# Kernel tuning notes

Measured on AMD Instinct MI355X. Metric: run time of the kernel, lower is better.

## Reference

```python
import jax, jax.numpy as jnp
import numpy as np

NUM_REQS = 8192
MAX_NUM_REQS = 16384
NUM_TOKENS = 16_777_216
MAX_CTX = 32768


def setup_inputs() -> dict:
    key = jax.random.key(0)
    k1, k2, k3 = jax.random.split(key, 3)
    # cumulative query start offsets: sorted, qsl[0]=0, qsl[-1]=NUM_TOKENS
    inner = jnp.sort(jax.random.randint(k1, (NUM_REQS - 1,), 0, NUM_TOKENS, dtype=jnp.int32))
    query_start_loc = jnp.concatenate([
        jnp.zeros((1,), jnp.int32), inner, jnp.full((1,), NUM_TOKENS, jnp.int32)
    ])
    idx_mapping = jax.random.randint(k2, (NUM_REQS,), 0, MAX_NUM_REQS, dtype=jnp.int32)
    num_computed_tokens = jax.random.randint(k3, (MAX_NUM_REQS,), 0, MAX_CTX, dtype=jnp.int32)
    pos = jnp.zeros((NUM_TOKENS,), jnp.int32)       # output buffer
    seq_lens = jnp.zeros((MAX_NUM_REQS,), jnp.int32)  # output buffer
    return {
        "idx_mapping": idx_mapping,
        "query_start_loc": query_start_loc,
        "num_computed_tokens": num_computed_tokens,
        "pos": pos,
        "seq_lens": seq_lens,
    }


def reference(idx_mapping, query_start_loc, num_computed_tokens, pos, seq_lens):
    num_reqs = idx_mapping.shape[0]            # static
    max_num_reqs = seq_lens.shape[0]           # static
    num_tokens = pos.shape[0]                  # static; == query_start_loc[-1] by construction

    # per-request query lengths and gathered computed-token counts
    query_lens = query_start_loc[1:] - query_start_loc[:-1]      # [num_reqs]
    nct = num_computed_tokens[idx_mapping]                       # [num_reqs]

    # seq_lens: [0:num_reqs] = nct + query_len, [num_reqs:] = 0
    seq_lens_out = jnp.zeros((max_num_reqs,), seq_lens.dtype).at[:num_reqs].set(
        (nct + query_lens).astype(seq_lens.dtype)
    )

    # pos: for each token t, find its owning request via searchsorted over
    # the ragged offsets, then pos[t] = nct[req] + (t - start[req]).
    t = jnp.arange(num_tokens, dtype=query_start_loc.dtype)      # [num_tokens]
    req = jnp.searchsorted(query_start_loc, t, side="right") - 1 # [num_tokens]
    req = jnp.clip(req, 0, num_reqs - 1)
    pos_out = (nct[req] + (t - query_start_loc[req])).astype(pos.dtype)

    return pos_out, seq_lens_out
```

## Files before the change

### kernel.cpp

```cpp
#include <hip/hip_runtime.h>


#define TPB 256
#define TILE_TOK 1024
#define SEQ_PER_BLOCK (TPB * 4)

typedef int vint4 __attribute__((ext_vector_type(4)));

__global__ __launch_bounds__(TPB) void fused_kernel(
    const int* __restrict__ idx_mapping,
    const int* __restrict__ qsl,
    const int* __restrict__ nct,
    int* __restrict__ pos_out,
    int* __restrict__ seq_out,
    int num_reqs, int max_num_reqs, int num_tokens,
    int pos_blocks)
{
    int b = blockIdx.x;

    if (b >= pos_blocks) {
        int i = (b - pos_blocks) * SEQ_PER_BLOCK + (int)threadIdx.x * 4;
        if (i >= max_num_reqs) return;
        vint4 v;
        #pragma unroll
        for (int k = 0; k < 4; ++k) {
            int idx = i + k;
            int val = 0;
            if (idx < num_reqs)
                val = nct[idx_mapping[idx]] + (qsl[idx + 1] - qsl[idx]);
            v[k] = val;
        }
        if (i + 4 <= max_num_reqs) {
            *(vint4*)(seq_out + i) = v;
        } else {
            for (int k = 0; k < max_num_reqs - i; ++k) seq_out[i + k] = v[k];
        }
        return;
    }

    int t = b * TILE_TOK + (int)threadIdx.x * 4;
    int tc = (t < num_tokens) ? t : (num_tokens - 1);

    int l = 0, h = num_reqs + 1;
    while (h - l > 1) {
        int mid = (l + h) >> 1;
        if (qsl[mid] <= tc) l = mid; else h = mid;
    }
    int r = l;
    int next = qsl[r + 1];
    int base = nct[idx_mapping[r]] - qsl[r];

    vint4 v;
    #pragma unroll
    for (int k = 0; k < 4; ++k) {
        int tk = t + k;
        while (tk >= next && r < num_reqs - 1) {
            ++r;
            next = qsl[r + 1];
            base = nct[idx_mapping[r]] - qsl[r];
        }
        v[k] = base + tk;
    }

    if (t + 4 <= num_tokens) {
        __builtin_nontemporal_store(v, (vint4*)(pos_out + t));
    } else {
        for (int k = 0; k < num_tokens - t; ++k) pos_out[t + k] = v[k];
    }
}

extern "C" void kernel_launch(void* const* d_in, const int* in_sizes, int n_in,
                              void* d_out, int out_size, void* d_ws, size_t ws_size,
                              hipStream_t stream) {
    const int* idx_mapping = (const int*)d_in[0];
    const int* qsl         = (const int*)d_in[1];
    const int* nct         = (const int*)d_in[2];

    int num_reqs     = in_sizes[0];
    int max_num_reqs = in_sizes[2];
    int num_tokens   = in_sizes[3];

    int* out = (int*)d_out;
    int* pos_out = out;
    int* seq_out = out + num_tokens;

    int pos_blocks = (int)(((long long)num_tokens + TILE_TOK - 1) / TILE_TOK);
    int seq_blocks = (max_num_reqs + SEQ_PER_BLOCK - 1) / SEQ_PER_BLOCK;

    fused_kernel<<<dim3(pos_blocks + seq_blocks), dim3(TPB), 0, stream>>>(
        idx_mapping, qsl, nct, pos_out, seq_out,
        num_reqs, max_num_reqs, num_tokens, pos_blocks);
}
```

Baseline: 142.2 us.

## Assign one block per request and drop per-token binary search

Work for the pos output is now split per request instead of per fixed token tile. Each block reads its request's start, end and base offset once, then strides over that request's tokens with aligned vector nontemporal stores, plus scalar head and tail stores. This removes the dependent binary search over query_start_loc that every thread ran, and the inner request-advance loop. In exchange, blocks get uneven amounts of work because request lengths vary, and misaligned head and tail elements use scalar stores.

```diff
diff --git a/kernel.cpp b/kernel.cpp
--- a/kernel.cpp
+++ b/kernel.cpp
@@ -2,7 +2,6 @@
 
 
 #define TPB 256
-#define TILE_TOK 1024
 #define SEQ_PER_BLOCK (TPB * 4)
 
 typedef int vint4 __attribute__((ext_vector_type(4)));
@@ -13,13 +12,13 @@
     const int* __restrict__ nct,
     int* __restrict__ pos_out,
     int* __restrict__ seq_out,
-    int num_reqs, int max_num_reqs, int num_tokens,
-    int pos_blocks)
+    int num_reqs, int max_num_reqs)
 {
     int b = blockIdx.x;
+    int tid = (int)threadIdx.x;
 
-    if (b >= pos_blocks) {
-        int i = (b - pos_blocks) * SEQ_PER_BLOCK + (int)threadIdx.x * 4;
+    if (b >= num_reqs) {
+        int i = (b - num_reqs) * SEQ_PER_BLOCK + tid * 4;
         if (i >= max_num_reqs) return;
         vint4 v;
         #pragma unroll
@@ -38,35 +37,25 @@
         return;
     }
 
-    int t = b * TILE_TOK + (int)threadIdx.x * 4;
-    int tc = (t < num_tokens) ? t : (num_tokens - 1);
+    int r = b;
+    int start = qsl[r];
+    int end   = qsl[r + 1];
+    if (start >= end) return;
+    int base  = nct[idx_mapping[r]] - start;
 
-    int l = 0, h = num_reqs + 1;
-    while (h - l > 1) {
-        int mid = (l + h) >> 1;
-        if (qsl[mid] <= tc) l = mid; else h = mid;
-    }
-    int r = l;
-    int next = qsl[r + 1];
-    int base = nct[idx_mapping[r]] - qsl[r];
+    int a = (start + 3) & ~3;
+    if (a > end) a = end;
+    if (tid < a - start) pos_out[start + tid] = base + start + tid;
 
-    vint4 v;
-    #pragma unroll
-    for (int k = 0; k < 4; ++k) {
-        int tk = t + k;
-        while (tk >= next && r < num_reqs - 1) {
-            ++r;
-            next = qsl[r + 1];
-            base = nct[idx_mapping[r]] - qsl[r];
-        }
-        v[k] = base + tk;
+    int e4 = a + ((end - a) & ~3);
+    for (int t = a + tid * 4; t < e4; t += TPB * 4) {
+        vint4 v;
+        v[0] = base + t;     v[1] = base + t + 1;
+        v[2] = base + t + 2; v[3] = base + t + 3;
+        __builtin_nontemporal_store(v, (vint4*)(pos_out + t));
     }
 
-    if (t + 4 <= num_tokens) {
-        __builtin_nontemporal_store(v, (vint4*)(pos_out + t));
-    } else {
-        for (int k = 0; k < num_tokens - t; ++k) pos_out[t + k] = v[k];
-    }
+    if (tid < end - e4) pos_out[e4 + tid] = base + e4 + tid;
 }
 
 extern "C" void kernel_launch(void* const* d_in, const int* in_sizes, int n_in,
@@ -84,10 +73,8 @@
     int* pos_out = out;
     int* seq_out = out + num_tokens;
 
-    int pos_blocks = (int)(((long long)num_tokens + TILE_TOK - 1) / TILE_TOK);
     int seq_blocks = (max_num_reqs + SEQ_PER_BLOCK - 1) / SEQ_PER_BLOCK;
 
-    fused_kernel<<<dim3(pos_blocks + seq_blocks), dim3(TPB), 0, stream>>>(
-        idx_mapping, qsl, nct, pos_out, seq_out,
-        num_reqs, max_num_reqs, num_tokens, pos_blocks);
+    fused_kernel<<<dim3(num_reqs + seq_blocks), dim3(TPB), 0, stream>>>(
+        idx_mapping, qsl, nct, pos_out, seq_out, num_reqs, max_num_reqs);
 }
```

Result: faster. 120.2 us (-15.5%).

## Do one binary search per block and write pos segment-by-segment per request

Applied to the files above, without the earlier changes.

Each block now covers 8192 tokens and performs a single binary search on the tile start, replacing one search per thread. It then walks the requests overlapping the tile and writes each segment cooperatively, with aligned vector stores and scalar heads and tails. This removes the redundant per-thread searches and the gathers that go with them. In exchange there are fewer blocks, and a sequential per-segment loop whose trip count depends on how many requests fall inside a tile.

```diff
diff --git a/kernel.cpp b/kernel.cpp
--- a/kernel.cpp
+++ b/kernel.cpp
@@ -2,7 +2,7 @@
 
 
 #define TPB 256
-#define TILE_TOK 1024
+#define TILE_TOK 8192
 #define SEQ_PER_BLOCK (TPB * 4)
 
 typedef int vint4 __attribute__((ext_vector_type(4)));
@@ -17,9 +17,10 @@
     int pos_blocks)
 {
     int b = blockIdx.x;
+    int tid = (int)threadIdx.x;
 
     if (b >= pos_blocks) {
-        int i = (b - pos_blocks) * SEQ_PER_BLOCK + (int)threadIdx.x * 4;
+        int i = (b - pos_blocks) * SEQ_PER_BLOCK + tid * 4;
         if (i >= max_num_reqs) return;
         vint4 v;
         #pragma unroll
@@ -38,34 +39,39 @@
         return;
     }
 
-    int t = b * TILE_TOK + (int)threadIdx.x * 4;
-    int tc = (t < num_tokens) ? t : (num_tokens - 1);
+    long long lo_l = (long long)b * TILE_TOK;
+    if (lo_l >= num_tokens) return;
+    int lo = (int)lo_l;
+    int hi = (int)(lo_l + TILE_TOK > (long long)num_tokens ? num_tokens
+                                                          : lo_l + TILE_TOK);
 
     int l = 0, h = num_reqs + 1;
     while (h - l > 1) {
         int mid = (l + h) >> 1;
-        if (qsl[mid] <= tc) l = mid; else h = mid;
+        if (qsl[mid] <= lo) l = mid; else h = mid;
     }
     int r = l;
-    int next = qsl[r + 1];
-    int base = nct[idx_mapping[r]] - qsl[r];
 
-    vint4 v;
-    #pragma unroll
-    for (int k = 0; k < 4; ++k) {
-        int tk = t + k;
-        while (tk >= next && r < num_reqs - 1) {
-            ++r;
-            next = qsl[r + 1];
-            base = nct[idx_mapping[r]] - qsl[r];
+    int seg_lo = lo;
+    while (seg_lo < hi) {
+        int q1 = qsl[r + 1];
+        int seg_hi = (q1 < hi) ? q1 : hi;
+        if (seg_hi > seg_lo) {
+            int base = nct[idx_mapping[r]] - qsl[r];
+            int a = (seg_lo + 3) & ~3;
+            if (a > seg_hi) a = seg_hi;
+            if (tid < a - seg_lo) pos_out[seg_lo + tid] = base + seg_lo + tid;
+            int e4 = a + ((seg_hi - a) & ~3);
+            for (int t = a + tid * 4; t < e4; t += TPB * 4) {
+                vint4 v;
+                v[0] = base + t;     v[1] = base + t + 1;
+                v[2] = base + t + 2; v[3] = base + t + 3;
+                __builtin_nontemporal_store(v, (vint4*)(pos_out + t));
+            }
+            if (tid < seg_hi - e4) pos_out[e4 + tid] = base + e4 + tid;
         }
-        v[k] = base + tk;
-    }
-
-    if (t + 4 <= num_tokens) {
-        __builtin_nontemporal_store(v, (vint4*)(pos_out + t));
-    } else {
-        for (int k = 0; k < num_tokens - t; ++k) pos_out[t + k] = v[k];
+        seg_lo = seg_hi;
+        ++r;
     }
 }
 
```

New measurement: 122.6 us. -13.8%, faster.
